# Optimization experiments

Measured on AMD Instinct MI355X. Metric: run time of the kernel, lower is better.

The kernel has to match this reference:

```python
import jax, jax.numpy as jnp
import numpy as np

D_MODEL = 512
DK = 4
DV = 8
HIDD = 10
HEAD = D_MODEL // DV  # 64
LN_EPS = 1e-5


def setup_inputs() -> dict:
    key = jax.random.key(0)
    ks = jax.random.split(key, 10)
    B, S, Se = 8, 512, 512
    u = jax.random.uniform  # torch.rand initializer for attention weights
    n = jax.random.normal
    return {
        "x": n(ks[0], (B, S, D_MODEL), jnp.float32),
        "x_enc": n(ks[1], (B, Se, D_MODEL), jnp.float32),
        "WqM": u(ks[2], (D_MODEL, HEAD * DK), jnp.float32),
        "WkM": u(ks[3], (D_MODEL, HEAD * DK), jnp.float32),
        "WvM": u(ks[4], (D_MODEL, HEAD * DV), jnp.float32),
        "ln_g": jnp.ones((D_MODEL,), jnp.float32),
        "ln_b": jnp.zeros((D_MODEL,), jnp.float32),
        "fc1_w": n(ks[5], (HIDD, D_MODEL), jnp.float32) * (1.0 / np.sqrt(D_MODEL)),
        "fc1_b": jnp.zeros((HIDD,), jnp.float32),
        "fc2_w": n(ks[6], (D_MODEL, HIDD), jnp.float32) * (1.0 / np.sqrt(HIDD)),
        "fc2_b": jnp.zeros((D_MODEL,), jnp.float32),
    }


def _attention(Xq, Xkv, WqM, WkM, WvM, causal_mul_mask):
    # NOTE: cross-attention in the source also uses WqM/WkM/WvM (Wq/Wk/Wv unused).
    B, Sq, _ = Xq.shape
    Sk = Xkv.shape[1]
    Q = (Xq @ WqM).reshape(B, Sq, HEAD, DK)
    K = (Xkv @ WkM).reshape(B, Sk, HEAD, DK)
    V = (Xkv @ WvM).reshape(B, Sk, HEAD, DV)
    score = jnp.einsum('bqhd,bkhd->bhqk', Q, K) / np.sqrt(DK).astype(np.float32)
    if causal_mul_mask:
        # Faithful quirk: multiplicative tril mask on scores (NOT additive -inf).
        score = score * jnp.tril(jnp.ones((Sq, Sk), score.dtype))
    w = jax.nn.softmax(score, axis=-1)
    out = jnp.einsum('bhqk,bkhd->bqhd', w, V)
    return out.reshape(B, Sq, HEAD * DV)  # HEAD*DV == d_model


def _layernorm(x, g, b):
    mu = jnp.mean(x, axis=-1, keepdims=True)
    var = jnp.mean(jnp.square(x - mu), axis=-1, keepdims=True)
    return (x - mu) * jax.lax.rsqrt(var + LN_EPS) * g + b


def reference(x, x_enc, WqM, WkM, WvM, ln_g, ln_b, fc1_w, fc1_b, fc2_w, fc2_b):
    fx = _attention(x, x, WqM, WkM, WvM, causal_mul_mask=True)
    fx = _attention(fx, x_enc, WqM, WkM, WvM, causal_mul_mask=False)
    y = _layernorm(x + fx, ln_g, ln_b)
    h = jax.nn.relu(y @ fc1_w.T + fc1_b)
    return h @ fc2_w.T + fc2_b
```

## Files before the change

kernel.cpp:

```cpp
#include <hip/hip_runtime.h>
#include <math.h>

#define D_MODEL 512
#define BATCH 8
#define SEQ 512
#define HEAD 64
#define DK 4
#define DV 8
#define HIDD 10

#define MR 32
#define KC 32
#define NC 256

__global__ __launch_bounds__(256) void proj_kernel(
    const float* __restrict__ xq, const float* __restrict__ xkv,
    const float* __restrict__ Wq, const float* __restrict__ Wk,
    const float* __restrict__ Wv,
    float* __restrict__ Q2, float* __restrict__ K2, float* __restrict__ V2)
{
    __shared__ float xt[KC * MR];
    __shared__ float wt[KC * NC];

    const int t  = threadIdx.x;
    const int bj = blockIdx.x & 3;
    const int br = blockIdx.x >> 2;
    const int r0 = br * MR;

    const float* X; const float* W; int ldw; int c0;
    if (bj == 0)      { X = xq;  W = Wq; ldw = 256; c0 = 0;   }
    else if (bj == 1) { X = xkv; W = Wk; ldw = 256; c0 = 0;   }
    else if (bj == 2) { X = xkv; W = Wv; ldw = 512; c0 = 0;   }
    else              { X = xkv; W = Wv; ldw = 512; c0 = 256; }

    const int rg = t >> 6;
    const int cq = t & 63;
    const int rs = t & 31;
    const int kq = t >> 5;

    float4 acc[8];
#pragma unroll
    for (int r = 0; r < 8; ++r) acc[r] = make_float4(0.f, 0.f, 0.f, 0.f);

    for (int kc = 0; kc < D_MODEL; kc += KC) {
        const float4 xa = *(const float4*)(X + (long)(r0 + rs) * D_MODEL + kc + kq * 4);
        xt[(kq * 4 + 0) * MR + rs] = xa.x;
        xt[(kq * 4 + 1) * MR + rs] = xa.y;
        xt[(kq * 4 + 2) * MR + rs] = xa.z;
        xt[(kq * 4 + 3) * MR + rs] = xa.w;

#pragma unroll
        for (int i = 0; i < 8; ++i) {
            const int row = i * 4 + rg;
            *(float4*)(wt + row * NC + cq * 4) =
                *(const float4*)(W + (long)(kc + row) * ldw + c0 + cq * 4);
        }
        __syncthreads();

#pragma unroll 4
        for (int k = 0; k < KC; ++k) {
            const float4 w4 = *(const float4*)(wt + k * NC + cq * 4);
            const float4 x0 = *(const float4*)(xt + k * MR + rg * 8);
            const float4 x1 = *(const float4*)(xt + k * MR + rg * 8 + 4);
            const float xr[8] = {x0.x, x0.y, x0.z, x0.w, x1.x, x1.y, x1.z, x1.w};
#pragma unroll
            for (int r = 0; r < 8; ++r) {
                acc[r].x = fmaf(xr[r], w4.x, acc[r].x);
                acc[r].y = fmaf(xr[r], w4.y, acc[r].y);
                acc[r].z = fmaf(xr[r], w4.z, acc[r].z);
                acc[r].w = fmaf(xr[r], w4.w, acc[r].w);
            }
        }
        __syncthreads();
    }

    const int b = r0 >> 9;
    const int sb = (r0 & 511) + rg * 8;
    if (bj <= 1) {
        float* dst = (bj == 0) ? Q2 : K2;
#pragma unroll
        for (int r = 0; r < 8; ++r)
            *(float4*)(dst + (((long)b * HEAD + cq) * SEQ + sb + r) * 4) = acc[r];
    } else {
        const int col = c0 + cq * 4;
        const int h = col >> 3;
        const int off = col & 7;
#pragma unroll
        for (int r = 0; r < 8; ++r)
            *(float4*)(V2 + (((long)b * HEAD + h) * SEQ + sb + r) * 8 + off) = acc[r];
    }
}

__global__ __launch_bounds__(256) void attn_kernel(
    const float* __restrict__ Q2, const float* __restrict__ K2,
    const float* __restrict__ V2, float* __restrict__ O, int causal)
{
    extern __shared__ float smem[];
    float* Kl = smem;
    float* Vl = smem + SEQ * DK;
    float* cs = Vl + SEQ * DV;

    const int t = threadIdx.x;
    const int bh = blockIdx.x >> 1;
    const int qhalf = blockIdx.x & 1;
    const int b = bh >> 6;
    const int h = bh & 63;

    const float4* Ks = (const float4*)(K2 + (long)bh * SEQ * DK);
    ((float4*)Kl)[t]       = Ks[t];
    ((float4*)Kl)[t + 256] = Ks[t + 256];
    const float4* Vs = (const float4*)(V2 + (long)bh * SEQ * DV);
#pragma unroll
    for (int i = 0; i < 4; ++i)
        ((float4*)Vl)[t + i * 256] = Vs[t + i * 256];
    __syncthreads();

    if (causal) {
        const int ch = t >> 3, d = t & 7;
        float s16 = 0.f;
#pragma unroll
        for (int i = 0; i < 16; ++i) s16 += Vl[(ch * 16 + i) * 8 + d];
        cs[ch * 8 + d] = s16;
        __syncthreads();
        if (t < 8) {
            cs[256 + t] = 0.f;
            float run = 0.f;
            for (int c2 = 31; c2 >= 0; --c2) {
                run += cs[c2 * 8 + t];
                cs[c2 * 8 + t] = run;
            }
        }
        __syncthreads();
    }

    const int q = qhalf * 256 + t;
    const float4 qv = *(const float4*)(Q2 + ((long)bh * SEQ + q) * 4);
    const float q0 = qv.x * 0.5f, q1 = qv.y * 0.5f;
    const float q2 = qv.z * 0.5f, q3 = qv.w * 0.5f;

    const int bound = causal ? q : (SEQ - 1);

    float m = -INFINITY, l = 0.f;
    float a0=0.f,a1=0.f,a2=0.f,a3=0.f,a4=0.f,a5=0.f,a6=0.f,a7=0.f;

    int s0 = 0;
    for (; s0 + 8 <= bound + 1; s0 += 8) {
        float sc[8];
#pragma unroll
        for (int i = 0; i < 8; ++i) {
            const float4 k4 = *(const float4*)(Kl + (s0 + i) * 4);
            sc[i] = fmaf(q0, k4.x, fmaf(q1, k4.y, fmaf(q2, k4.z, q3 * k4.w)));
        }
        float gm = fmaxf(fmaxf(fmaxf(sc[0], sc[1]), fmaxf(sc[2], sc[3])),
                         fmaxf(fmaxf(sc[4], sc[5]), fmaxf(sc[6], sc[7])));
        if (gm > m) {
            float scale = __expf(m - gm);
            l *= scale;
            a0*=scale; a1*=scale; a2*=scale; a3*=scale;
            a4*=scale; a5*=scale; a6*=scale; a7*=scale;
            m = gm;
        }
#pragma unroll
        for (int i = 0; i < 8; ++i) {
            float p = __expf(sc[i] - m);
            l += p;
            const float4 v0 = *(const float4*)(Vl + (s0 + i) * 8);
            const float4 v1 = *(const float4*)(Vl + (s0 + i) * 8 + 4);
            a0 = fmaf(p, v0.x, a0); a1 = fmaf(p, v0.y, a1);
            a2 = fmaf(p, v0.z, a2); a3 = fmaf(p, v0.w, a3);
            a4 = fmaf(p, v1.x, a4); a5 = fmaf(p, v1.y, a5);
            a6 = fmaf(p, v1.z, a6); a7 = fmaf(p, v1.w, a7);
        }
    }
    for (int s = s0; s <= bound; ++s) {
        const float4 k4 = *(const float4*)(Kl + s * 4);
        float sc = fmaf(q0, k4.x, fmaf(q1, k4.y, fmaf(q2, k4.z, q3 * k4.w)));
        if (sc > m) {
            float scale = __expf(m - sc);
            l *= scale;
            a0*=scale; a1*=scale; a2*=scale; a3*=scale;
            a4*=scale; a5*=scale; a6*=scale; a7*=scale;
            m = sc;
        }
        float p = __expf(sc - m);
        l += p;
        const float4 v0 = *(const float4*)(Vl + s * 8);
        const float4 v1 = *(const float4*)(Vl + s * 8 + 4);
        a0 = fmaf(p, v0.x, a0); a1 = fmaf(p, v0.y, a1);
        a2 = fmaf(p, v0.z, a2); a3 = fmaf(p, v0.w, a3);
        a4 = fmaf(p, v1.x, a4); a5 = fmaf(p, v1.y, a5);
        a6 = fmaf(p, v1.z, a6); a7 = fmaf(p, v1.w, a7);
    }

    if (causal && q < SEQ - 1) {
        float M = fmaxf(m, 0.f);
        float scale = __expf(m - M);
        float pm = __expf(-M);
        l = l * scale + pm * (float)(SEQ - 1 - q);
        int nq = q + 1;
        int cq2 = nq >> 4;
        float sv[8];
#pragma unroll
        for (int d = 0; d < 8; ++d) sv[d] = cs[(cq2 + 1) * 8 + d];
        for (int s = nq; s < (cq2 + 1) * 16; ++s) {
            const float4 v0 = *(const float4*)(Vl + s * 8);
            const float4 v1 = *(const float4*)(Vl + s * 8 + 4);
            sv[0]+=v0.x; sv[1]+=v0.y; sv[2]+=v0.z; sv[3]+=v0.w;
            sv[4]+=v1.x; sv[5]+=v1.y; sv[6]+=v1.z; sv[7]+=v1.w;
        }
        a0 = a0*scale + pm*sv[0]; a1 = a1*scale + pm*sv[1];
        a2 = a2*scale + pm*sv[2]; a3 = a3*scale + pm*sv[3];
        a4 = a4*scale + pm*sv[4]; a5 = a5*scale + pm*sv[5];
        a6 = a6*scale + pm*sv[6]; a7 = a7*scale + pm*sv[7];
    }

    float inv = 1.0f / l;
    const long obase = (long)b * SEQ * 512 + (long)q * 512 + h * DV;
    *(float4*)(O + obase)     = make_float4(a0*inv, a1*inv, a2*inv, a3*inv);
    *(float4*)(O + obase + 4) = make_float4(a4*inv, a5*inv, a6*inv, a7*inv);
}

__global__ __launch_bounds__(256) void ln_mlp_kernel(
    const float* __restrict__ x, const float* __restrict__ fx,
    const float* __restrict__ g, const float* __restrict__ beta,
    const float* __restrict__ w1, const float* __restrict__ b1,
    const float* __restrict__ w2, const float* __restrict__ b2,
    float* __restrict__ out)
{
    const int t = threadIdx.x;
    const int lane = t & 63;
    const int row = blockIdx.x * 4 + (t >> 6);
    const long base = (long)row * D_MODEL;
    const int e0 = lane * 8;

    const float4 xa = *(const float4*)(x + base + e0);
    const float4 xb = *(const float4*)(x + base + e0 + 4);
    const float4 fa = *(const float4*)(fx + base + e0);
    const float4 fb = *(const float4*)(fx + base + e0 + 4);
    float z[8] = {xa.x+fa.x, xa.y+fa.y, xa.z+fa.z, xa.w+fa.w,
                  xb.x+fb.x, xb.y+fb.y, xb.z+fb.z, xb.w+fb.w};

    float sum = 0.f;
#pragma unroll
    for (int j = 0; j < 8; ++j) sum += z[j];
#pragma unroll
    for (int o = 32; o > 0; o >>= 1) sum += __shfl_xor(sum, o);
    float mu = sum * (1.0f / 512.0f);

    float d[8], ss = 0.f;
#pragma unroll
    for (int j = 0; j < 8; ++j) { d[j] = z[j] - mu; ss += d[j] * d[j]; }
#pragma unroll
    for (int o = 32; o > 0; o >>= 1) ss += __shfl_xor(ss, o);
    float rs = rsqrtf(ss * (1.0f / 512.0f) + 1e-5f);

    const float4 ga = *(const float4*)(g + e0);
    const float4 gb = *(const float4*)(g + e0 + 4);
    const float4 ba = *(const float4*)(beta + e0);
    const float4 bb = *(const float4*)(beta + e0 + 4);
    const float gg[8] = {ga.x,ga.y,ga.z,ga.w,gb.x,gb.y,gb.z,gb.w};
    const float bt[8] = {ba.x,ba.y,ba.z,ba.w,bb.x,bb.y,bb.z,bb.w};
    float y[8];
#pragma unroll
    for (int j = 0; j < 8; ++j) y[j] = d[j] * rs * gg[j] + bt[j];

    float part[HIDD];
#pragma unroll
    for (int i = 0; i < HIDD; ++i) {
        const float4 wa = *(const float4*)(w1 + i * 512 + e0);
        const float4 wb = *(const float4*)(w1 + i * 512 + e0 + 4);
        part[i] = y[0]*wa.x + y[1]*wa.y + y[2]*wa.z + y[3]*wa.w
                + y[4]*wb.x + y[5]*wb.y + y[6]*wb.z + y[7]*wb.w;
    }
#pragma unroll
    for (int i = 0; i < HIDD; ++i)
#pragma unroll
        for (int o = 32; o > 0; o >>= 1) part[i] += __shfl_xor(part[i], o);

    float hv[HIDD];
#pragma unroll
    for (int i = 0; i < HIDD; ++i) hv[i] = fmaxf(part[i] + b1[i], 0.f);

    float o8[8];
#pragma unroll
    for (int j = 0; j < 8; ++j) o8[j] = b2[e0 + j];
#pragma unroll
    for (int i = 0; i < HIDD; ++i)
#pragma unroll
        for (int j = 0; j < 8; ++j)
            o8[j] = fmaf(hv[i], w2[(long)(e0 + j) * 10 + i], o8[j]);

    *(float4*)(out + base + e0)     = make_float4(o8[0], o8[1], o8[2], o8[3]);
    *(float4*)(out + base + e0 + 4) = make_float4(o8[4], o8[5], o8[6], o8[7]);
}

extern "C" void kernel_launch(void* const* d_in, const int* in_sizes, int n_in,
                              void* d_out, int out_size, void* d_ws, size_t ws_size,
                              hipStream_t stream) {
    (void)in_sizes; (void)n_in; (void)out_size; (void)ws_size;
    const float* x    = (const float*)d_in[0];
    const float* xenc = (const float*)d_in[1];
    const float* Wq   = (const float*)d_in[2];
    const float* Wk   = (const float*)d_in[3];
    const float* Wv   = (const float*)d_in[4];
    const float* ln_g = (const float*)d_in[5];
    const float* ln_b = (const float*)d_in[6];
    const float* w1   = (const float*)d_in[7];
    const float* b1   = (const float*)d_in[8];
    const float* w2   = (const float*)d_in[9];
    const float* b2   = (const float*)d_in[10];
    float* out = (float*)d_out;

    float* ws = (float*)d_ws;
    float* Q2 = ws;
    float* K2 = Q2 + 1048576;
    float* V2 = K2 + 1048576;
    float* A  = V2 + 2097152;

    const int nrows = BATCH * SEQ;
    const size_t lds_cross  = (size_t)(SEQ * DK + SEQ * DV) * 4;
    const size_t lds_causal = lds_cross + (size_t)(33 * DV) * 4;
    const int proj_grid = (nrows / MR) * 4;

    proj_kernel<<<dim3(proj_grid), 256, 0, stream>>>(x, x, Wq, Wk, Wv, Q2, K2, V2);
    attn_kernel<<<dim3(BATCH * HEAD * 2), 256, lds_causal, stream>>>(Q2, K2, V2, A, 1);

    proj_kernel<<<dim3(proj_grid), 256, 0, stream>>>(A, xenc, Wq, Wk, Wv, Q2, K2, V2);
    attn_kernel<<<dim3(BATCH * HEAD * 2), 256, lds_cross, stream>>>(Q2, K2, V2, A, 0);

    ln_mlp_kernel<<<dim3(nrows / 4), 256, 0, stream>>>(x, A, ln_g, ln_b,
                                                       w1, b1, w2, b2, out);
}
```

Baseline: 341.9 us.

## Split attention over key halves, merge partials, fuse cross K/V projection

Restructures the whole pipeline. One projection kernel now computes Q/K/V for self-attention plus K/V for cross-attention from x_enc, using smaller column tiles for more blocks. Attention is split into two key halves per query with flash-style partial (m, l, acc) outputs. A combine kernel merges them for the causal pass, and the LN/MLP kernel merges them directly for the cross pass. The second Q projection is split-K into two buffers that are summed on load, exp is switched to exp2 with prescaled queries, and the causal mask is applied multiplicatively over the full range instead of the suffix-sum trick. This raises parallelism and occupancy, but adds partial-buffer traffic, an extra kernel, and masked work that the old kernel skipped analytically.

```diff
diff --git a/kernel.cpp b/kernel.cpp
--- a/kernel.cpp
+++ b/kernel.cpp
@@ -11,36 +11,44 @@
 
 #define MR 32
 #define KC 32
-#define NC 256
-
-__global__ __launch_bounds__(256) void proj_kernel(
-    const float* __restrict__ xq, const float* __restrict__ xkv,
+#define NC 128
+
+__device__ __forceinline__ float4 fma4(float s, float4 w, float4 a) {
+    a.x = fmaf(s, w.x, a.x); a.y = fmaf(s, w.y, a.y);
+    a.z = fmaf(s, w.z, a.z); a.w = fmaf(s, w.w, a.w);
+    return a;
+}
+
+__global__ __launch_bounds__(256, 8) void proj_kernel(
+    const float* __restrict__ x, const float* __restrict__ xe,
     const float* __restrict__ Wq, const float* __restrict__ Wk,
     const float* __restrict__ Wv,
-    float* __restrict__ Q2, float* __restrict__ K2, float* __restrict__ V2)
+    float* __restrict__ Q1, float* __restrict__ K1, float* __restrict__ V1,
+    float* __restrict__ Kc, float* __restrict__ Vc)
 {
     __shared__ float xt[KC * MR];
     __shared__ float wt[KC * NC];
 
     const int t  = threadIdx.x;
-    const int bj = blockIdx.x & 3;
-    const int br = blockIdx.x >> 2;
+    const int bj = blockIdx.x >> 7;
+    const int br = blockIdx.x & 127;
     const int r0 = br * MR;
 
-    const float* X; const float* W; int ldw; int c0;
-    if (bj == 0)      { X = xq;  W = Wq; ldw = 256; c0 = 0;   }
-    else if (bj == 1) { X = xkv; W = Wk; ldw = 256; c0 = 0;   }
-    else if (bj == 2) { X = xkv; W = Wv; ldw = 512; c0 = 0;   }
-    else              { X = xkv; W = Wv; ldw = 512; c0 = 256; }
-
-    const int rg = t >> 6;
-    const int cq = t & 63;
+    const float* X; const float* W; int ldw; int c0; float* dst; int vtype;
+    if (bj < 2)       { X = x;  W = Wq; ldw = 256; c0 = bj * 128;         dst = Q1; vtype = 0; }
+    else if (bj < 4)  { X = x;  W = Wk; ldw = 256; c0 = (bj - 2) * 128;   dst = K1; vtype = 0; }
+    else if (bj < 8)  { X = x;  W = Wv; ldw = 512; c0 = (bj - 4) * 128;   dst = V1; vtype = 1; }
+    else if (bj < 10) { X = xe; W = Wk; ldw = 256; c0 = (bj - 8) * 128;   dst = Kc; vtype = 0; }
+    else              { X = xe; W = Wv; ldw = 512; c0 = (bj - 10) * 128;  dst = Vc; vtype = 1; }
+
+    const int cq = t & 31;
+    const int rr = t >> 5;
     const int rs = t & 31;
     const int kq = t >> 5;
 
-    float4 acc[8];
-#pragma unroll
-    for (int r = 0; r < 8; ++r) acc[r] = make_float4(0.f, 0.f, 0.f, 0.f);
+    float4 acc[4];
+#pragma unroll
+    for (int r = 0; r < 4; ++r) acc[r] = make_float4(0.f, 0.f, 0.f, 0.f);
 
     for (int kc = 0; kc < D_MODEL; kc += KC) {
         const float4 xa = *(const float4*)(X + (long)(r0 + rs) * D_MODEL + kc + kq * 4);
@@ -50,178 +58,209 @@
         xt[(kq * 4 + 3) * MR + rs] = xa.w;
 
 #pragma unroll
-        for (int i = 0; i < 8; ++i) {
-            const int row = i * 4 + rg;
-            *(float4*)(wt + row * NC + cq * 4) =
-                *(const float4*)(W + (long)(kc + row) * ldw + c0 + cq * 4);
+        for (int i = 0; i < 4; ++i) {
+            const int row = i * 8 + (t >> 5);
+            *(float4*)(wt + row * NC + (t & 31) * 4) =
+                *(const float4*)(W + (long)(kc + row) * ldw + c0 + (t & 31) * 4);
         }
         __syncthreads();
 
 #pragma unroll 4
         for (int k = 0; k < KC; ++k) {
             const float4 w4 = *(const float4*)(wt + k * NC + cq * 4);
-            const float4 x0 = *(const float4*)(xt + k * MR + rg * 8);
-            const float4 x1 = *(const float4*)(xt + k * MR + rg * 8 + 4);
-            const float xr[8] = {x0.x, x0.y, x0.z, x0.w, x1.x, x1.y, x1.z, x1.w};
-#pragma unroll
-            for (int r = 0; r < 8; ++r) {
-                acc[r].x = fmaf(xr[r], w4.x, acc[r].x);
-                acc[r].y = fmaf(xr[r], w4.y, acc[r].y);
-                acc[r].z = fmaf(xr[r], w4.z, acc[r].z);
-                acc[r].w = fmaf(xr[r], w4.w, acc[r].w);
-            }
+            const float4 x4 = *(const float4*)(xt + k * MR + rr * 4);
+            acc[0] = fma4(x4.x, w4, acc[0]);
+            acc[1] = fma4(x4.y, w4, acc[1]);
+            acc[2] = fma4(x4.z, w4, acc[2]);
+            acc[3] = fma4(x4.w, w4, acc[3]);
         }
         __syncthreads();
     }
 
-    const int b = r0 >> 9;
-    const int sb = (r0 & 511) + rg * 8;
-    if (bj <= 1) {
-        float* dst = (bj == 0) ? Q2 : K2;
-#pragma unroll
-        for (int r = 0; r < 8; ++r)
-            *(float4*)(dst + (((long)b * HEAD + cq) * SEQ + sb + r) * 4) = acc[r];
+    const int b  = r0 >> 9;
+    const int sb = (r0 & 511) + rr * 4;
+    if (vtype == 0) {
+        const int h = (c0 >> 2) + cq;
+#pragma unroll
+        for (int r = 0; r < 4; ++r)
+            *(float4*)(dst + (((long)b * HEAD + h) * SEQ + sb + r) * 4) = acc[r];
     } else {
         const int col = c0 + cq * 4;
         const int h = col >> 3;
-        const int off = col & 7;
-#pragma unroll
-        for (int r = 0; r < 8; ++r)
-            *(float4*)(V2 + (((long)b * HEAD + h) * SEQ + sb + r) * 8 + off) = acc[r];
-    }
-}
-
-__global__ __launch_bounds__(256) void attn_kernel(
-    const float* __restrict__ Q2, const float* __restrict__ K2,
-    const float* __restrict__ V2, float* __restrict__ O, int causal)
-{
-    extern __shared__ float smem[];
-    float* Kl = smem;
-    float* Vl = smem + SEQ * DK;
-    float* cs = Vl + SEQ * DV;
-
-    const int t = threadIdx.x;
-    const int bh = blockIdx.x >> 1;
-    const int qhalf = blockIdx.x & 1;
-    const int b = bh >> 6;
-    const int h = bh & 63;
-
-    const float4* Ks = (const float4*)(K2 + (long)bh * SEQ * DK);
-    ((float4*)Kl)[t]       = Ks[t];
-    ((float4*)Kl)[t + 256] = Ks[t + 256];
-    const float4* Vs = (const float4*)(V2 + (long)bh * SEQ * DV);
-#pragma unroll
-    for (int i = 0; i < 4; ++i)
-        ((float4*)Vl)[t + i * 256] = Vs[t + i * 256];
+        const int off = col & 4;
+#pragma unroll
+        for (int r = 0; r < 4; ++r)
+            *(float4*)(dst + (((long)b * HEAD + h) * SEQ + sb + r) * 8 + off) = acc[r];
+    }
+}
+
+__global__ __launch_bounds__(256, 8) void proj2_kernel(
+    const float* __restrict__ A, const float* __restrict__ Wq,
+    float* __restrict__ Qa, float* __restrict__ Qb)
+{
+    __shared__ float xt[KC * MR];
+    __shared__ float wt[KC * 64];
+
+    const int t  = threadIdx.x;
+    const int kh = blockIdx.x & 1;
+    const int bj = (blockIdx.x >> 1) & 3;
+    const int br = blockIdx.x >> 3;
+    const int r0 = br * MR;
+    const int c0 = bj * 64;
+    const int kb = kh * 256;
+    float* dst = kh ? Qb : Qa;
+
+    const int cq = t & 15;
+    const int rr = t >> 4;
+    const int rs = t & 31, kq = t >> 5;
+
+    float4 acc[2];
+    acc[0] = make_float4(0.f, 0.f, 0.f, 0.f);
+    acc[1] = acc[0];
+
+    for (int kc = 0; kc < 256; kc += KC) {
+        const float4 xa = *(const float4*)(A + (long)(r0 + rs) * D_MODEL + kb + kc + kq * 4);
+        xt[(kq * 4 + 0) * MR + rs] = xa.x;
+        xt[(kq * 4 + 1) * MR + rs] = xa.y;
+        xt[(kq * 4 + 2) * MR + rs] = xa.z;
+        xt[(kq * 4 + 3) * MR + rs] = xa.w;
+#pragma unroll
+        for (int i = 0; i < 2; ++i) {
+            const int row = i * 16 + (t >> 4);
+            *(float4*)(wt + row * 64 + (t & 15) * 4) =
+                *(const float4*)(Wq + (long)(kb + kc + row) * 256 + c0 + (t & 15) * 4);
+        }
+        __syncthreads();
+#pragma unroll 4
+        for (int k = 0; k < KC; ++k) {
+            const float4 w4 = *(const float4*)(wt + k * 64 + cq * 4);
+            const float2 x2 = *(const float2*)(xt + k * MR + rr * 2);
+            acc[0] = fma4(x2.x, w4, acc[0]);
+            acc[1] = fma4(x2.y, w4, acc[1]);
+        }
+        __syncthreads();
+    }
+
+    const int b  = r0 >> 9;
+    const int sb = (r0 & 511) + rr * 2;
+    const int h  = (c0 >> 2) + cq;
+#pragma unroll
+    for (int r = 0; r < 2; ++r)
+        *(float4*)(dst + (((long)b * HEAD + h) * SEQ + sb + r) * 4) = acc[r];
+}
+
+template <bool MASKED>
+__device__ __forceinline__ void attn_scan(
+    const float* __restrict__ Kl, const float* __restrict__ Vl, const int qb,
+    const float q0, const float q1, const float q2, const float q3,
+    float& m, float& l, float (&a)[8])
+{
+    for (int s0 = 0; s0 < 256; s0 += 8) {
+        float sc[8];
+#pragma unroll
+        for (int i = 0; i < 8; ++i) {
+            const float4 k4 = *(const float4*)(Kl + (s0 + i) * DK);
+            const float d = fmaf(q0, k4.x, fmaf(q1, k4.y, fmaf(q2, k4.z, q3 * k4.w)));
+            sc[i] = (MASKED && (s0 + i) > qb) ? 0.f : d;
+        }
+        const float gm = fmaxf(fmaxf(fmaxf(sc[0], sc[1]), fmaxf(sc[2], sc[3])),
+                               fmaxf(fmaxf(sc[4], sc[5]), fmaxf(sc[6], sc[7])));
+        if (gm > m) {
+            const float scale = __builtin_amdgcn_exp2f(m - gm);
+            l *= scale;
+#pragma unroll
+            for (int r = 0; r < 8; ++r) a[r] *= scale;
+            m = gm;
+        }
+#pragma unroll
+        for (int i = 0; i < 8; ++i) {
+            const float p = __builtin_amdgcn_exp2f(sc[i] - m);
+            l += p;
+            const float4 v0 = *(const float4*)(Vl + (s0 + i) * DV);
+            const float4 v1 = *(const float4*)(Vl + (s0 + i) * DV + 4);
+            a[0] = fmaf(p, v0.x, a[0]); a[1] = fmaf(p, v0.y, a[1]);
+            a[2] = fmaf(p, v0.z, a[2]); a[3] = fmaf(p, v0.w, a[3]);
+            a[4] = fmaf(p, v1.x, a[4]); a[5] = fmaf(p, v1.y, a[5]);
+            a[6] = fmaf(p, v1.z, a[6]); a[7] = fmaf(p, v1.w, a[7]);
+        }
+    }
+}
+
+__global__ __launch_bounds__(256, 8) void attn_kernel(
+    const float* __restrict__ Qa, const float* __restrict__ Qb,
+    const float* __restrict__ K2, const float* __restrict__ V2,
+    float* __restrict__ PA, float* __restrict__ PM, const int causal)
+{
+    __shared__ float Kl[256 * DK];
+    __shared__ float Vl[256 * DV];
+
+    const int t  = threadIdx.x;
+    const int bh = blockIdx.x >> 2;
+    const int qh = (blockIdx.x >> 1) & 1;
+    const int kh = blockIdx.x & 1;
+
+    ((float4*)Kl)[t] = ((const float4*)(K2 + ((long)bh * SEQ + kh * 256) * DK))[t];
+    const float4* Vs = (const float4*)(V2 + ((long)bh * SEQ + kh * 256) * DV);
+    ((float4*)Vl)[t]       = Vs[t];
+    ((float4*)Vl)[t + 256] = Vs[t + 256];
+
+    const int q = qh * 256 + t;
+    float4 qv = *(const float4*)(Qa + ((long)bh * SEQ + q) * DK);
+    if (Qb) {
+        const float4 qw = *(const float4*)(Qb + ((long)bh * SEQ + q) * DK);
+        qv.x += qw.x; qv.y += qw.y; qv.z += qw.z; qv.w += qw.w;
+    }
+    const float cf = 0.5f * 1.44269504088896340736f;
+    const float q0 = qv.x * cf, q1 = qv.y * cf, q2 = qv.z * cf, q3 = qv.w * cf;
+
     __syncthreads();
 
-    if (causal) {
-        const int ch = t >> 3, d = t & 7;
-        float s16 = 0.f;
-#pragma unroll
-        for (int i = 0; i < 16; ++i) s16 += Vl[(ch * 16 + i) * 8 + d];
-        cs[ch * 8 + d] = s16;
-        __syncthreads();
-        if (t < 8) {
-            cs[256 + t] = 0.f;
-            float run = 0.f;
-            for (int c2 = 31; c2 >= 0; --c2) {
-                run += cs[c2 * 8 + t];
-                cs[c2 * 8 + t] = run;
-            }
-        }
-        __syncthreads();
-    }
-
-    const int q = qhalf * 256 + t;
-    const float4 qv = *(const float4*)(Q2 + ((long)bh * SEQ + q) * 4);
-    const float q0 = qv.x * 0.5f, q1 = qv.y * 0.5f;
-    const float q2 = qv.z * 0.5f, q3 = qv.w * 0.5f;
-
-    const int bound = causal ? q : (SEQ - 1);
-
-    float m = -INFINITY, l = 0.f;
-    float a0=0.f,a1=0.f,a2=0.f,a3=0.f,a4=0.f,a5=0.f,a6=0.f,a7=0.f;
-
-    int s0 = 0;
-    for (; s0 + 8 <= bound + 1; s0 += 8) {
-        float sc[8];
-#pragma unroll
-        for (int i = 0; i < 8; ++i) {
-            const float4 k4 = *(const float4*)(Kl + (s0 + i) * 4);
-            sc[i] = fmaf(q0, k4.x, fmaf(q1, k4.y, fmaf(q2, k4.z, q3 * k4.w)));
-        }
-        float gm = fmaxf(fmaxf(fmaxf(sc[0], sc[1]), fmaxf(sc[2], sc[3])),
-                         fmaxf(fmaxf(sc[4], sc[5]), fmaxf(sc[6], sc[7])));
-        if (gm > m) {
-            float scale = __expf(m - gm);
-            l *= scale;
-            a0*=scale; a1*=scale; a2*=scale; a3*=scale;
-            a4*=scale; a5*=scale; a6*=scale; a7*=scale;
-            m = gm;
-        }
-#pragma unroll
-        for (int i = 0; i < 8; ++i) {
-            float p = __expf(sc[i] - m);
-            l += p;
-            const float4 v0 = *(const float4*)(Vl + (s0 + i) * 8);
-            const float4 v1 = *(const float4*)(Vl + (s0 + i) * 8 + 4);
-            a0 = fmaf(p, v0.x, a0); a1 = fmaf(p, v0.y, a1);
-            a2 = fmaf(p, v0.z, a2); a3 = fmaf(p, v0.w, a3);
-            a4 = fmaf(p, v1.x, a4); a5 = fmaf(p, v1.y, a5);
-            a6 = fmaf(p, v1.z, a6); a7 = fmaf(p, v1.w, a7);
-        }
-    }
-    for (int s = s0; s <= bound; ++s) {
-        const float4 k4 = *(const float4*)(Kl + s * 4);
-        float sc = fmaf(q0, k4.x, fmaf(q1, k4.y, fmaf(q2, k4.z, q3 * k4.w)));
-        if (sc > m) {
-            float scale = __expf(m - sc);
-            l *= scale;
-            a0*=scale; a1*=scale; a2*=scale; a3*=scale;
-            a4*=scale; a5*=scale; a6*=scale; a7*=scale;
-            m = sc;
-        }
-        float p = __expf(sc - m);
-        l += p;
-        const float4 v0 = *(const float4*)(Vl + s * 8);
-        const float4 v1 = *(const float4*)(Vl + s * 8 + 4);
-        a0 = fmaf(p, v0.x, a0); a1 = fmaf(p, v0.y, a1);
-        a2 = fmaf(p, v0.z, a2); a3 = fmaf(p, v0.w, a3);
-        a4 = fmaf(p, v1.x, a4); a5 = fmaf(p, v1.y, a5);
-        a6 = fmaf(p, v1.z, a6); a7 = fmaf(p, v1.w, a7);
-    }
-
-    if (causal && q < SEQ - 1) {
-        float M = fmaxf(m, 0.f);
-        float scale = __expf(m - M);
-        float pm = __expf(-M);
-        l = l * scale + pm * (float)(SEQ - 1 - q);
-        int nq = q + 1;
-        int cq2 = nq >> 4;
-        float sv[8];
-#pragma unroll
-        for (int d = 0; d < 8; ++d) sv[d] = cs[(cq2 + 1) * 8 + d];
-        for (int s = nq; s < (cq2 + 1) * 16; ++s) {
-            const float4 v0 = *(const float4*)(Vl + s * 8);
-            const float4 v1 = *(const float4*)(Vl + s * 8 + 4);
-            sv[0]+=v0.x; sv[1]+=v0.y; sv[2]+=v0.z; sv[3]+=v0.w;
-            sv[4]+=v1.x; sv[5]+=v1.y; sv[6]+=v1.z; sv[7]+=v1.w;
-        }
-        a0 = a0*scale + pm*sv[0]; a1 = a1*scale + pm*sv[1];
-        a2 = a2*scale + pm*sv[2]; a3 = a3*scale + pm*sv[3];
-        a4 = a4*scale + pm*sv[4]; a5 = a5*scale + pm*sv[5];
-        a6 = a6*scale + pm*sv[6]; a7 = a7*scale + pm*sv[7];
-    }
-
-    float inv = 1.0f / l;
-    const long obase = (long)b * SEQ * 512 + (long)q * 512 + h * DV;
-    *(float4*)(O + obase)     = make_float4(a0*inv, a1*inv, a2*inv, a3*inv);
-    *(float4*)(O + obase + 4) = make_float4(a4*inv, a5*inv, a6*inv, a7*inv);
+    float m = -INFINITY, l = 0.f, a[8];
+#pragma unroll
+    for (int r = 0; r < 8; ++r) a[r] = 0.f;
+
+    if (causal)
+        attn_scan<true >(Kl, Vl, q - kh * 256, q0, q1, q2, q3, m, l, a);
+    else
+        attn_scan<false>(Kl, Vl, 255,          q0, q1, q2, q3, m, l, a);
+
+    const long p = ((long)(bh * 2 + kh)) * SEQ + q;
+    *(float4*)(PA + p * 8)     = make_float4(a[0], a[1], a[2], a[3]);
+    *(float4*)(PA + p * 8 + 4) = make_float4(a[4], a[5], a[6], a[7]);
+    *(float2*)(PM + p * 2)     = make_float2(m, l);
+}
+
+__global__ __launch_bounds__(256) void combine_kernel(
+    const float* __restrict__ PA, const float* __restrict__ PM,
+    float* __restrict__ A)
+{
+    const int tid = blockIdx.x * 256 + threadIdx.x;
+    const int bh  = tid >> 9;
+    const int q   = tid & 511;
+    const long p0 = ((long)bh * 2 + 0) * SEQ + q;
+    const long p1 = ((long)bh * 2 + 1) * SEQ + q;
+    const float2 ml0 = *(const float2*)(PM + p0 * 2);
+    const float2 ml1 = *(const float2*)(PM + p1 * 2);
+    const float M  = fmaxf(ml0.x, ml1.x);
+    float w0 = __builtin_amdgcn_exp2f(ml0.x - M);
+    float w1 = __builtin_amdgcn_exp2f(ml1.x - M);
+    const float inv = 1.0f / fmaf(ml0.y, w0, ml1.y * w1);
+    w0 *= inv; w1 *= inv;
+    const float4 x0 = *(const float4*)(PA + p0 * 8);
+    const float4 x1 = *(const float4*)(PA + p0 * 8 + 4);
+    const float4 y0 = *(const float4*)(PA + p1 * 8);
+    const float4 y1 = *(const float4*)(PA + p1 * 8 + 4);
+    const int b = bh >> 6, h = bh & 63;
+    float* dst = A + ((long)b * SEQ + q) * D_MODEL + h * DV;
+    *(float4*)(dst)     = make_float4(x0.x*w0 + y0.x*w1, x0.y*w0 + y0.y*w1,
+                                      x0.z*w0 + y0.z*w1, x0.w*w0 + y0.w*w1);
+    *(float4*)(dst + 4) = make_float4(x1.x*w0 + y1.x*w1, x1.y*w0 + y1.y*w1,
+                                      x1.z*w0 + y1.z*w1, x1.w*w0 + y1.w*w1);
 }
 
 __global__ __launch_bounds__(256) void ln_mlp_kernel(
-    const float* __restrict__ x, const float* __restrict__ fx,
+    const float* __restrict__ x,
+    const float* __restrict__ PA, const float* __restrict__ PM,
     const float* __restrict__ g, const float* __restrict__ beta,
     const float* __restrict__ w1, const float* __restrict__ b1,
     const float* __restrict__ w2, const float* __restrict__ b2,
@@ -230,29 +269,45 @@
     const int t = threadIdx.x;
     const int lane = t & 63;
     const int row = blockIdx.x * 4 + (t >> 6);
+    const int b = row >> 9, q = row & 511;
     const long base = (long)row * D_MODEL;
     const int e0 = lane * 8;
 
+    const long p0 = (((long)b * HEAD + lane) * 2 + 0) * SEQ + q;
+    const long p1 = (((long)b * HEAD + lane) * 2 + 1) * SEQ + q;
+    const float2 ml0 = *(const float2*)(PM + p0 * 2);
+    const float2 ml1 = *(const float2*)(PM + p1 * 2);
+    const float M  = fmaxf(ml0.x, ml1.x);
+    float cw0 = __builtin_amdgcn_exp2f(ml0.x - M);
+    float cw1 = __builtin_amdgcn_exp2f(ml1.x - M);
+    const float inv = 1.0f / fmaf(ml0.y, cw0, ml1.y * cw1);
+    cw0 *= inv; cw1 *= inv;
+    const float4 fa0 = *(const float4*)(PA + p0 * 8);
+    const float4 fa1 = *(const float4*)(PA + p0 * 8 + 4);
+    const float4 fb0 = *(const float4*)(PA + p1 * 8);
+    const float4 fb1 = *(const float4*)(PA + p1 * 8 + 4);
+
     const float4 xa = *(const float4*)(x + base + e0);
     const float4 xb = *(const float4*)(x + base + e0 + 4);
-    const float4 fa = *(const float4*)(fx + base + e0);
-    const float4 fb = *(const float4*)(fx + base + e0 + 4);
-    float z[8] = {xa.x+fa.x, xa.y+fa.y, xa.z+fa.z, xa.w+fa.w,
-                  xb.x+fb.x, xb.y+fb.y, xb.z+fb.z, xb.w+fb.w};
+    float z[8] = {
+        xa.x + fa0.x*cw0 + fb0.x*cw1, xa.y + fa0.y*cw0 + fb0.y*cw1,
+        xa.z + fa0.z*cw0 + fb0.z*cw1, xa.w + fa0.w*cw0 + fb0.w*cw1,
+        xb.x + fa1.x*cw0 + fb1.x*cw1, xb.y + fa1.y*cw0 + fb1.y*cw1,
+        xb.z + fa1.z*cw0 + fb1.z*cw1, xb.w + fa1.w*cw0 + fb1.w*cw1};
 
     float sum = 0.f;
 #pragma unroll
     for (int j = 0; j < 8; ++j) sum += z[j];
 #pragma unroll
     for (int o = 32; o > 0; o >>= 1) sum += __shfl_xor(sum, o);
-    float mu = sum * (1.0f / 512.0f);
+    const float mu = sum * (1.0f / 512.0f);
 
     float d[8], ss = 0.f;
 #pragma unroll
     for (int j = 0; j < 8; ++j) { d[j] = z[j] - mu; ss += d[j] * d[j]; }
 #pragma unroll
     for (int o = 32; o > 0; o >>= 1) ss += __shfl_xor(ss, o);
-    float rs = rsqrtf(ss * (1.0f / 512.0f) + 1e-5f);
+    const float rs = rsqrtf(ss * (1.0f / 512.0f) + 1e-5f);
 
     const float4 ga = *(const float4*)(g + e0);
     const float4 gb = *(const float4*)(g + e0 + 4);
@@ -281,14 +336,21 @@
 #pragma unroll
     for (int i = 0; i < HIDD; ++i) hv[i] = fmaxf(part[i] + b1[i], 0.f);
 
-    float o8[8];
-#pragma unroll
-    for (int j = 0; j < 8; ++j) o8[j] = b2[e0 + j];
-#pragma unroll
-    for (int i = 0; i < HIDD; ++i)
-#pragma unroll
-        for (int j = 0; j < 8; ++j)
-            o8[j] = fmaf(hv[i], w2[(long)(e0 + j) * 10 + i], o8[j]);
+    const float4 b2a = *(const float4*)(b2 + e0);
+    const float4 b2b = *(const float4*)(b2 + e0 + 4);
+    float o8[8] = {b2a.x,b2a.y,b2a.z,b2a.w,b2b.x,b2b.y,b2b.z,b2b.w};
+#pragma unroll
+    for (int j = 0; j < 8; ++j) {
+        const float* wr = w2 + (long)(e0 + j) * 10;
+        const float2 wA = *(const float2*)(wr);
+        const float2 wB = *(const float2*)(wr + 2);
+        const float2 wC = *(const float2*)(wr + 4);
+        const float2 wD = *(const float2*)(wr + 6);
+        const float2 wE = *(const float2*)(wr + 8);
+        o8[j] += hv[0]*wA.x + hv[1]*wA.y + hv[2]*wB.x + hv[3]*wB.y
+               + hv[4]*wC.x + hv[5]*wC.y + hv[6]*wD.x + hv[7]*wD.y
+               + hv[8]*wE.x + hv[9]*wE.y;
+    }
 
     *(float4*)(out + base + e0)     = make_float4(o8[0], o8[1], o8[2], o8[3]);
     *(float4*)(out + base + e0 + 4) = make_float4(o8[4], o8[5], o8[6], o8[7]);
@@ -312,22 +374,23 @@
     float* out = (float*)d_out;
 
     float* ws = (float*)d_ws;
-    float* Q2 = ws;
-    float* K2 = Q2 + 1048576;
-    float* V2 = K2 + 1048576;
-    float* A  = V2 + 2097152;
-
-    const int nrows = BATCH * SEQ;
-    const size_t lds_cross  = (size_t)(SEQ * DK + SEQ * DV) * 4;
-    const size_t lds_causal = lds_cross + (size_t)(33 * DV) * 4;
-    const int proj_grid = (nrows / MR) * 4;
-
-    proj_kernel<<<dim3(proj_grid), 256, 0, stream>>>(x, x, Wq, Wk, Wv, Q2, K2, V2);
-    attn_kernel<<<dim3(BATCH * HEAD * 2), 256, lds_causal, stream>>>(Q2, K2, V2, A, 1);
-
-    proj_kernel<<<dim3(proj_grid), 256, 0, stream>>>(A, xenc, Wq, Wk, Wv, Q2, K2, V2);
-    attn_kernel<<<dim3(BATCH * HEAD * 2), 256, lds_cross, stream>>>(Q2, K2, V2, A, 0);
-
-    ln_mlp_kernel<<<dim3(nrows / 4), 256, 0, stream>>>(x, A, ln_g, ln_b,
-                                                       w1, b1, w2, b2, out);
-}
+    float* Q1 = ws;
+    float* K1 = ws + 1048576;
+    float* V1 = ws + 2097152;
+    float* Kc = ws + 4194304;
+    float* Vc = ws + 5242880;
+    float* PA = ws + 7340032;
+    float* PM = ws + 11534336;
+    float* A  = K1;
+    float* Qa = Q1;
+    float* Qb = ws + 3145728;
+
+    proj_kernel<<<dim3(1792), 256, 0, stream>>>(x, xenc, Wq, Wk, Wv,
+                                                Q1, K1, V1, Kc, Vc);
+    attn_kernel<<<dim3(2048), 256, 0, stream>>>(Q1, nullptr, K1, V1, PA, PM, 1);
+    combine_kernel<<<dim3(1024), 256, 0, stream>>>(PA, PM, A);
+    proj2_kernel<<<dim3(1024), 256, 0, stream>>>(A, Wq, Qa, Qb);
+    attn_kernel<<<dim3(2048), 256, 0, stream>>>(Qa, Qb, Kc, Vc, PA, PM, 0);
+    ln_mlp_kernel<<<dim3(1024), 256, 0, stream>>>(x, PA, PM, ln_g, ln_b,
+                                                  w1, b1, w2, b2, out);
+}
```

Measured after the change: 350.6 us. +2.6%, slower.
